# Optimization experiments

Measured on AMD Instinct MI355X. Metric: run time of the kernel, lower is better.

Reference implementation:

```python
import jax, jax.numpy as jnp
import numpy as np

B, H0, W0, C = 8, 56, 56, 256
KC = VC = C
HID = 4 * C
NH = 8  # ChannelAttention default num_heads


def _ln(x, g, b, eps=1e-5):
    m = x.mean(-1, keepdims=True)
    v = jnp.var(x, axis=-1, keepdims=True)
    return (x - m) * jax.lax.rsqrt(v + eps) * g + b


def _dwconv(x, w, b, H, W):
    # x: [B, N, C] -> depthwise 3x3 on [B, C, H, W]
    Bn, N, Cc = x.shape
    t = x.transpose(0, 2, 1).reshape(Bn, Cc, H, W)
    y = jax.lax.conv_general_dilated(t, w, (1, 1), 'SAME', feature_group_count=Cc,
                                     dimension_numbers=('NCHW', 'OIHW', 'NCHW'))
    y = y + b[None, :, None, None]
    return y.reshape(Bn, Cc, H * W).transpose(0, 2, 1)


def _mixffn(x, H, W, w1, b1, dww, dwb, lg, lb, w2, b2):
    f = x @ w1.T + b1  # fc1(x), reused for the skip (torch computes it twice, same value)
    ax = jax.nn.gelu(_ln(_dwconv(f, dww, dwb, H, W) + f, lg, lb), approximate=False)
    return ax @ w2.T + b2


def _eff_attn(xn, kw, kb, qw, qb, vw, vb, rw, rb):
    # 1x1 convs == per-pixel linear; head_count=1
    k = jax.nn.softmax(xn @ kw.T + kb, axis=1)  # softmax over spatial N
    q = jax.nn.softmax(xn @ qw.T + qb, axis=2)  # softmax over key channels
    v = xn @ vw.T + vb
    ctx = jnp.einsum('bnk,bnv->bkv', k, v)      # [B, KC, VC]
    att = jnp.einsum('bkv,bnk->bnv', ctx, q)    # [B, N, VC]
    return att @ rw.T + rb


def _chan_attn(xn, temp, qkv_w, pw, pb):
    Bn, N, Cc = xn.shape
    d = Cc // NH
    qkv = (xn @ qkv_w.T).reshape(Bn, N, 3, NH, d).transpose(2, 0, 3, 4, 1)  # [3,B,h,d,N]
    q, k, v = qkv[0], qkv[1], qkv[2]
    q = q / jnp.maximum(jnp.linalg.norm(q, axis=-1, keepdims=True), 1e-12)
    k = k / jnp.maximum(jnp.linalg.norm(k, axis=-1, keepdims=True), 1e-12)
    attn = jax.nn.softmax(jnp.einsum('bhdn,bhen->bhde', q, k) * temp, axis=-1)  # [B,h,d,d]
    out = jnp.einsum('bhde,bhen->bhdn', attn, v).transpose(0, 3, 1, 2).reshape(Bn, N, Cc)
    return out @ pw.T + pb


def _forward(x, ln1g, ln1b, eakw, eakb, eaqw, eaqb, eavw, eavb, earw, earb,
             ln2g, ln2b, m1w1, m1b1, m1dww, m1dwb, m1lg, m1lb, m1w2, m1b2,
             ln3g, ln3b, catemp, caqkvw, capw, capb,
             ln4g, ln4b, m2w1, m2b1, m2dww, m2dwb, m2lg, m2lb, m2w2, m2b2, H, W):
    add1 = x + _eff_attn(_ln(x, ln1g, ln1b), eakw, eakb, eaqw, eaqb, eavw, eavb, earw, earb)
    add2 = add1 + _mixffn(_ln(add1, ln2g, ln2b), H, W, m1w1, m1b1, m1dww, m1dwb, m1lg, m1lb, m1w2, m1b2)
    add3 = add2 + _chan_attn(_ln(add2, ln3g, ln3b), catemp, caqkvw, capw, capb)
    return add3 + _mixffn(_ln(add3, ln4g, ln4b), H, W, m2w1, m2b1, m2dww, m2dwb, m2lg, m2lb, m2w2, m2b2)


def setup_inputs() -> dict:
    key = jax.random.key(0)
    ks = jax.random.split(key, 16)
    s = 0.02
    rn = lambda k, shape: jax.random.normal(k, shape, jnp.float32) * s
    f32 = jnp.float32
    return {
        'x': jax.random.normal(ks[0], (B, H0 * W0, C), f32),
        'H': H0, 'W': W0,
        'ln1g': jnp.ones(C, f32), 'ln1b': jnp.zeros(C, f32),
        'eakw': rn(ks[1], (KC, C)), 'eakb': jnp.zeros(KC, f32),
        'eaqw': rn(ks[2], (KC, C)), 'eaqb': jnp.zeros(KC, f32),
        'eavw': rn(ks[3], (VC, C)), 'eavb': jnp.zeros(VC, f32),
        'earw': rn(ks[4], (C, VC)), 'earb': jnp.zeros(C, f32),
        'ln2g': jnp.ones(C, f32), 'ln2b': jnp.zeros(C, f32),
        'm1w1': rn(ks[5], (HID, C)), 'm1b1': jnp.zeros(HID, f32),
        'm1dww': rn(ks[6], (HID, 1, 3, 3)), 'm1dwb': jnp.zeros(HID, f32),
        'm1lg': jnp.ones(HID, f32), 'm1lb': jnp.zeros(HID, f32),
        'm1w2': rn(ks[7], (C, HID)), 'm1b2': jnp.zeros(C, f32),
        'ln3g': jnp.ones(C, f32), 'ln3b': jnp.zeros(C, f32),
        'catemp': jnp.ones((NH, 1, 1), f32),
        'caqkvw': rn(ks[8], (3 * C, C)),
        'capw': rn(ks[9], (C, C)), 'capb': jnp.zeros(C, f32),
        'ln4g': jnp.ones(C, f32), 'ln4b': jnp.zeros(C, f32),
        'm2w1': rn(ks[10], (HID, C)), 'm2b1': jnp.zeros(HID, f32),
        'm2dww': rn(ks[11], (HID, 1, 3, 3)), 'm2dwb': jnp.zeros(HID, f32),
        'm2lg': jnp.ones(HID, f32), 'm2lb': jnp.zeros(HID, f32),
        'm2w2': rn(ks[12], (C, HID)), 'm2b2': jnp.zeros(C, f32),
    }


def reference(x, H, W, ln1g, ln1b, eakw, eakb, eaqw, eaqb, eavw, eavb, earw, earb,
              ln2g, ln2b, m1w1, m1b1, m1dww, m1dwb, m1lg, m1lb, m1w2, m1b2,
              ln3g, ln3b, catemp, caqkvw, capw, capb,
              ln4g, ln4b, m2w1, m2b1, m2dww, m2dwb, m2lg, m2lb, m2w2, m2b2):
    return _forward(x, ln1g, ln1b, eakw, eakb, eaqw, eaqb, eavw, eavb, earw, earb,
                    ln2g, ln2b, m1w1, m1b1, m1dww, m1dwb, m1lg, m1lb, m1w2, m1b2,
                    ln3g, ln3b, catemp, caqkvw, capw, capb,
                    ln4g, ln4b, m2w1, m2b1, m2dww, m2dwb, m2lg, m2lb, m2w2, m2b2, H, W)
```

## Files before the change

kernel.cpp:

```cpp
#include <hip/hip_runtime.h>
#include <hip/hip_bf16.h>

typedef __hip_bfloat16 bf16;
typedef __attribute__((ext_vector_type(8))) short short8;
typedef __attribute__((ext_vector_type(4))) float floatx4;

#define DI __device__ __forceinline__

DI unsigned short bfbits(float f){
    bf16 h = __float2bfloat16(f);
    return *reinterpret_cast<unsigned short*>(&h);
}
DI float bu(unsigned short u){
    union { unsigned int i; float f; } x; x.i = ((unsigned int)u) << 16; return x.f;
}

DI float gelu_exact(float x){
    float z = fabsf(x) * 0.70710678118654752f;
    float t = __builtin_amdgcn_rcpf(fmaf(0.3275911f, z, 1.f));
    float p = t * fmaf(t, fmaf(t, fmaf(t, fmaf(t, 1.061405429f, -1.453152027f),
                    1.421413741f), -0.284496736f), 0.254829592f);
    float e = __expf(-z*z);
    float er = fmaf(-p, e, 1.f);
    er = copysignf(er, x);
    return 0.5f * x * (1.f + er);
}

DI void gload16(const void* g, void* l){
    __builtin_amdgcn_global_load_lds(
        (const __attribute__((address_space(1))) unsigned int*)g,
        (__attribute__((address_space(3))) unsigned int*)l,
        16, 0, 0);
}

static constexpr int BATCH = 8;
static constexpr int HH = 56, WW = 56;
static constexpr int NPOS = HH * WW;
static constexpr int CDIM = 256;
static constexpr int HIDD = 1024;
static constexpr int MTOT = BATCH * NPOS;
static constexpr int NCHUNK = 49;
static constexpr int LP = 40;
static constexpr int TNS = 7;

struct WArgs {
    const float* src[10];
    bf16* dst[10];
    int n[10];
};
__global__ __launch_bounds__(256) void wcvt_kernel(WArgs a){
    int wid = blockIdx.y;
    int i = (blockIdx.x*256 + threadIdx.x) * 8;
    if (i >= a.n[wid]) return;
    const float* s = a.src[wid] + i;
    float4 f0 = *(const float4*)(s);
    float4 f1 = *(const float4*)(s + 4);
    union { uint4 u; unsigned short us[8]; } p;
    p.us[0]=bfbits(f0.x); p.us[1]=bfbits(f0.y); p.us[2]=bfbits(f0.z); p.us[3]=bfbits(f0.w);
    p.us[4]=bfbits(f1.x); p.us[5]=bfbits(f1.y); p.us[6]=bfbits(f1.z); p.us[7]=bfbits(f1.w);
    *(uint4*)(a.dst[wid] + i) = p.u;
}

__global__ __launch_bounds__(256) void wtrans_kernel(const float* __restrict__ w1, const float* __restrict__ w2,
                                                     float* __restrict__ t1, float* __restrict__ t2){
    int i = blockIdx.x*256 + threadIdx.x;
    const float* w = blockIdx.y ? w2 : w1;
    float* t = blockIdx.y ? t2 : t1;
    int tap = i >> 10, c = i & 1023;
    t[i] = w[c*9 + tap];
}

template<typename TC>
__global__ __launch_bounds__(256) void mfma_gemm(
    const bf16* __restrict__ A, const bf16* __restrict__ Bw,
    const float* __restrict__ bias, const float* __restrict__ addend,
    TC* __restrict__ C, int M, int N, int K, int lda,
    long long strA, long long strB, long long strC, long long strAdd)
{
    __shared__ __align__(16) float smemf[8192];
    short* S = (short*)smemf;
    int tid = threadIdx.x;
    int bz = blockIdx.z;
    A  += (long long)bz * strA;
    Bw += (long long)bz * strB;
    C  += (long long)bz * strC;
    if (addend) addend += (long long)bz * strAdd;

    int gx = gridDim.x;
    int nwg = gx * gridDim.y;
    int bidl = blockIdx.y * gx + blockIdx.x;
    int qq = nwg >> 3, rr = nwg & 7;
    int xcd = bidl & 7, ixx = bidl >> 3;
    int tile = (xcd < rr) ? (xcd*(qq+1) + ixx) : (rr*(qq+1) + (xcd-rr)*qq + ixx);
    int n0 = (tile % gx) * 128, m0 = (tile / gx) * 128;

    int w = tid >> 6, lane = tid & 63, lm = lane & 15, quad = lane >> 4;
    int mw = (w >> 1) * 64, nw = (w & 1) * 64;

    int c0 = w*128 + lane, c1 = c0 + 64;
    int ar0 = c0 >> 2, ac0 = (c0 & 3) ^ (ar0 & 3);
    int ar1 = c1 >> 2, ac1 = (c1 & 3) ^ (ar1 & 3);
    int rgA0 = m0 + ar0; if (rgA0 > M-1) rgA0 = M-1;
    int rgA1 = m0 + ar1; if (rgA1 > M-1) rgA1 = M-1;
    short* aL0 = S + (2*w+0)*512;
    short* aL1 = S + (2*w+1)*512;
    short* bL0 = S + 4096 + (2*w+0)*512;
    short* bL1 = S + 4096 + (2*w+1)*512;
    const bf16* Arow0 = A + (long long)rgA0*lda + ac0*8;
    const bf16* Arow1 = A + (long long)rgA1*lda + ac1*8;
    const bf16* Brow0 = Bw + (long long)(n0+ar0)*K + ac0*8;
    const bf16* Brow1 = Bw + (long long)(n0+ar1)*K + ac1*8;

    floatx4 z = {0.f, 0.f, 0.f, 0.f};
    floatx4 acc[4][4];
    #pragma unroll
    for (int mi = 0; mi < 4; mi++)
        #pragma unroll
        for (int ni = 0; ni < 4; ni++) acc[mi][ni] = z;

    int sq = quad ^ (lm & 3);

    auto STAGE = [&](int k0, int poff){
        gload16(Arow0 + k0, aL0 + poff);
        gload16(Arow1 + k0, aL1 + poff);
        gload16(Brow0 + k0, bL0 + poff);
        gload16(Brow1 + k0, bL1 + poff);
    };

    STAGE(0, 0);
    __syncthreads();
    int NS = K >> 5;
    for (int st = 0; st < NS; st++){
        int poff = (st & 1) << 13;
        if (st + 1 < NS) STAGE((st+1)*32, poff ^ 8192);
        short8 af[4], bfr[4];
        #pragma unroll
        for (int mi = 0; mi < 4; mi++)
            af[mi] = *(const short8*)&S[poff + (((mw + mi*16 + lm)<<2) + sq)*8];
        #pragma unroll
        for (int ni = 0; ni < 4; ni++)
            bfr[ni] = *(const short8*)&S[poff + 4096 + (((nw + ni*16 + lm)<<2) + sq)*8];
        #pragma unroll
        for (int mi = 0; mi < 4; mi++)
            #pragma unroll
            for (int ni = 0; ni < 4; ni++)
                acc[mi][ni] = __builtin_amdgcn_mfma_f32_16x16x32_bf16(af[mi], bfr[ni], acc[mi][ni], 0, 0, 0);
        __syncthreads();
    }

    float bvv[4];
    #pragma unroll
    for (int ni = 0; ni < 4; ni++)
        bvv[ni] = bias ? bias[n0 + nw + ni*16 + lm] : 0.f;
    float* esc = smemf + w*1088;
    int rl0 = lane >> 3;
    #pragma unroll
    for (int mi = 0; mi < 4; mi++){
        #pragma unroll
        for (int ni = 0; ni < 4; ni++)
            #pragma unroll
            for (int r = 0; r < 4; r++)
                esc[(quad*4 + r)*68 + ni*16 + lm] = acc[mi][ni][r] + bvv[ni];
        #pragma unroll
        for (int p = 0; p < 2; p++){
            int rloc = p*8 + rl0;
            int rg = m0 + mw + mi*16 + rloc;
            if (rg < M){
                if constexpr (sizeof(TC) == 2){
                    int cl = (lane & 7) * 8;
                    float4 u0 = *(const float4*)&esc[rloc*68 + cl];
                    float4 u1 = *(const float4*)&esc[rloc*68 + cl + 4];
                    if (addend){
                        long long ai = (long long)rg*N + (n0 + nw + cl);
                        float4 a0 = *(const float4*)(addend + ai);
                        float4 a1 = *(const float4*)(addend + ai + 4);
                        u0.x+=a0.x; u0.y+=a0.y; u0.z+=a0.z; u0.w+=a0.w;
                        u1.x+=a1.x; u1.y+=a1.y; u1.z+=a1.z; u1.w+=a1.w;
                    }
                    union { uint4 u; unsigned short us[8]; } pk;
                    pk.us[0]=bfbits(u0.x); pk.us[1]=bfbits(u0.y); pk.us[2]=bfbits(u0.z); pk.us[3]=bfbits(u0.w);
                    pk.us[4]=bfbits(u1.x); pk.us[5]=bfbits(u1.y); pk.us[6]=bfbits(u1.z); pk.us[7]=bfbits(u1.w);
                    *(uint4*)(C + (long long)rg*N + (n0 + nw + cl)) = pk.u;
                } else {
                    int cl4 = (lane & 7) * 4;
                    long long co = (long long)rg*N + (n0 + nw);
                    float4 u0 = *(const float4*)&esc[rloc*68 + cl4];
                    float4 u1 = *(const float4*)&esc[rloc*68 + 32 + cl4];
                    if (addend){
                        float4 a0 = *(const float4*)(addend + co + cl4);
                        float4 a1 = *(const float4*)(addend + co + 32 + cl4);
                        u0.x+=a0.x; u0.y+=a0.y; u0.z+=a0.z; u0.w+=a0.w;
                        u1.x+=a1.x; u1.y+=a1.y; u1.z+=a1.z; u1.w+=a1.w;
                    }
                    *(float4*)(C + co + cl4) = u0;
                    *(float4*)(C + co + 32 + cl4) = u1;
                }
            }
        }
    }
}

__global__ __launch_bounds__(256) void gemm_tn_mfma(const bf16* __restrict__ V, const bf16* __restrict__ Kb,
                                                    float* __restrict__ part){
    __shared__ short As[128*LP];
    __shared__ short Bs[128*LP];
    int tid = threadIdx.x;
    int bz = blockIdx.z;
    int b = bz / TNS, s = bz % TNS;
    const bf16* Vb = V  + (long long)b*NPOS*CDIM;
    const bf16* Kc = Kb + (long long)b*NPOS*CDIM;
    int m0 = blockIdx.y * 128, n0 = blockIdx.x * 128;
    int w = tid >> 6, lane = tid & 63, lm = lane & 15, quad = lane >> 4;
    int mw = (w >> 1) * 64, nw = (w & 1) * 64;

    floatx4 z = {0.f,0.f,0.f,0.f};
    floatx4 acc[4][4];
    #pragma unroll
    for (int mi = 0; mi < 4; mi++)
        #pragma unroll
        for (int ni = 0; ni < 4; ni++) acc[mi][ni] = z;

    int r = tid & 31, cgrp = tid >> 5;

    for (int step = 0; step < 448/32; step++){
        int nb = s*448 + step*32;
        #pragma unroll
        for (int cc = 0; cc < 2; cc++){
            int ch = cgrp*8 + cc*64;
            short8 va = *(const short8*)(Vb + (long long)(nb + r)*CDIM + m0 + ch);
            short8 ka = *(const short8*)(Kc + (long long)(nb + r)*CDIM + n0 + ch);
            #pragma unroll
            for (int i = 0; i < 8; i++){
                As[(ch+i)*LP + r] = va[i];
                Bs[(ch+i)*LP + r] = ka[i];
            }
        }
        __syncthreads();
        short8 af[4], bfr[4];
        #pragma unroll
        for (int mi = 0; mi < 4; mi++)
            af[mi] = *(const short8*)&As[(mw + mi*16 + lm)*LP + quad*8];
        #pragma unroll
        for (int ni = 0; ni < 4; ni++)
            bfr[ni] = *(const short8*)&Bs[(nw + ni*16 + lm)*LP + quad*8];
        #pragma unroll
        for (int mi = 0; mi < 4; mi++)
            #pragma unroll
            for (int ni = 0; ni < 4; ni++)
                acc[mi][ni] = __builtin_amdgcn_mfma_f32_16x16x32_bf16(af[mi], bfr[ni], acc[mi][ni], 0, 0, 0);
        __syncthreads();
    }

    float* pb = part + (long long)bz * CDIM * CDIM;
    #pragma unroll
    for (int ni = 0; ni < 4; ni++){
        int cg = n0 + nw + ni*16 + lm;
        #pragma unroll
        for (int mi = 0; mi < 4; mi++){
            #pragma unroll
            for (int rr = 0; rr < 4; rr++){
                int rg = m0 + mw + mi*16 + quad*4 + rr;
                pb[(long long)rg*CDIM + cg] = acc[mi][ni][rr];
            }
        }
    }
}

__global__ __launch_bounds__(256) void ctx_reduce(const float* __restrict__ part, bf16* __restrict__ ctxb){
    long long idx = (long long)blockIdx.x*256 + threadIdx.x;
    int b = (int)(idx >> 16);
    int rem = (int)(idx & 65535);
    float s = 0.f;
    #pragma unroll
    for (int sp = 0; sp < TNS; sp++)
        s += part[((long long)(b*TNS+sp) << 16) + rem];
    ctxb[idx] = __float2bfloat16(s);
}

DI void st4o(float* p, long long i, float a, float b, float c, float d){
    float4 v = make_float4(a,b,c,d); *(float4*)(p + i) = v;
}
DI void st4o(bf16* p, long long i, float a, float b, float c, float d){
    union { unsigned long long u; unsigned short us[4]; } pk;
    pk.us[0]=bfbits(a); pk.us[1]=bfbits(b); pk.us[2]=bfbits(c); pk.us[3]=bfbits(d);
    *(unsigned long long*)(p + i) = pk.u;
}
template<typename TOUT>
__global__ __launch_bounds__(256) void ln4_kernel(const float* __restrict__ x, const float* __restrict__ g,
                                                  const float* __restrict__ b, TOUT* __restrict__ y){
    int wv = threadIdx.x >> 6, lane = threadIdx.x & 63;
    long long row = (long long)blockIdx.x*4 + wv;
    float4 v = *(const float4*)(x + row*256 + lane*4);
    float s  = v.x + v.y + v.z + v.w;
    float ss = v.x*v.x + v.y*v.y + v.z*v.z + v.w*v.w;
    #pragma unroll
    for (int off = 32; off > 0; off >>= 1){
        s  += __shfl_down(s,  off);
        ss += __shfl_down(ss, off);
    }
    s = __shfl(s, 0); ss = __shfl(ss, 0);
    float mean = s * (1.f/256.f);
    float var  = ss * (1.f/256.f) - mean*mean;
    float inv  = rsqrtf(var + 1e-5f);
    float4 gv = *(const float4*)(g + lane*4);
    float4 bv = *(const float4*)(b + lane*4);
    st4o(y, row*256 + lane*4,
         (v.x-mean)*inv*gv.x + bv.x, (v.y-mean)*inv*gv.y + bv.y,
         (v.z-mean)*inv*gv.z + bv.z, (v.w-mean)*inv*gv.w + bv.w);
}

__global__ __launch_bounds__(256) void colsm_p1(const float* __restrict__ x, float* __restrict__ lmax, float* __restrict__ lsum){
    int b = blockIdx.x / NCHUNK, ch = blockIdx.x % NCHUNK;
    int c = threadIdx.x;
    const float* base = x + ((long long)b*NPOS + ch*64)*512 + c;
    float m = -1e30f;
    for (int r = 0; r < 64; r++) m = fmaxf(m, base[(long long)r*512]);
    float s = 0.f;
    for (int r = 0; r < 64; r++) s += expf(base[(long long)r*512] - m);
    lmax[(long long)blockIdx.x*CDIM + c] = m;
    lsum[(long long)blockIdx.x*CDIM + c] = s;
}
__global__ __launch_bounds__(256) void colsm_p2(const float* __restrict__ lmax, const float* __restrict__ lsum,
                                                float* __restrict__ gmax, float* __restrict__ ginv){
    int b = blockIdx.x; int c = threadIdx.x;
    float g = -1e30f;
    for (int ch = 0; ch < NCHUNK; ch++) g = fmaxf(g, lmax[((long long)b*NCHUNK+ch)*CDIM + c]);
    float s = 0.f;
    for (int ch = 0; ch < NCHUNK; ch++)
        s += lsum[((long long)b*NCHUNK+ch)*CDIM + c] * expf(lmax[((long long)b*NCHUNK+ch)*CDIM + c] - g);
    gmax[b*CDIM + c] = g; ginv[b*CDIM + c] = 1.f / s;
}
__global__ __launch_bounds__(256) void colsm_p3(const float* __restrict__ x, bf16* __restrict__ y,
                                                const float* __restrict__ gmax, const float* __restrict__ ginv){
    long long idx = (long long)blockIdx.x*256 + threadIdx.x;
    int c = (int)(idx & 255);
    long long row = idx >> 8;
    int b = (int)(row / NPOS);
    y[idx] = __float2bfloat16(expf(x[row*512 + c] - gmax[b*CDIM + c]) * ginv[b*CDIM + c]);
}

__global__ __launch_bounds__(256) void rowsm4b_kernel(const float* __restrict__ x, const float* __restrict__ bias,
                                                      bf16* __restrict__ y){
    int wv = threadIdx.x >> 6, lane = threadIdx.x & 63;
    long long row = (long long)blockIdx.x*4 + wv;
    float4 v = *(const float4*)(x + row*512 + 256 + lane*4);
    float4 bb = *(const float4*)(bias + lane*4);
    v.x += bb.x; v.y += bb.y; v.z += bb.z; v.w += bb.w;
    float m = fmaxf(fmaxf(v.x, v.y), fmaxf(v.z, v.w));
    #pragma unroll
    for (int off = 32; off > 0; off >>= 1) m = fmaxf(m, __shfl_down(m, off));
    m = __shfl(m, 0);
    float e0 = expf(v.x - m), e1 = expf(v.y - m), e2 = expf(v.z - m), e3 = expf(v.w - m);
    float s = e0 + e1 + e2 + e3;
    #pragma unroll
    for (int off = 32; off > 0; off >>= 1) s += __shfl_down(s, off);
    s = __shfl(s, 0);
    float inv = 1.f / s;
    st4o(y, row*256 + lane*4, e0*inv, e1*inv, e2*inv, e3*inv);
}

__global__ __launch_bounds__(256) void dwconv_ln_gelu_kernel(const bf16* __restrict__ f, const float* __restrict__ wT,
        const float* __restrict__ db, const float* __restrict__ lg, const float* __restrict__ lb, bf16* __restrict__ out){
    __shared__ short Ls[18*1024];
    int tid = threadIdx.x;
    int b = blockIdx.x & 7;
    int rem = blockIdx.x >> 3;
    int h = rem / 14, w0 = (rem % 14) * 4;
    const bf16* fb = f + (long long)b * NPOS * HIDD;

    #pragma unroll
    for (int j = 0; j < 9; j++){
        int idx = j*256 + tid;
        int rc = idx >> 7, chunk = idx & 127;
        int row = rc / 6, col = rc % 6;
        int hy = h - 1 + row, wx = w0 - 1 + col;
        uint4 v = {0,0,0,0};
        if (hy >= 0 && hy < HH && wx >= 0 && wx < WW)
            v = *(const uint4*)(fb + (long long)(hy*WW + wx)*HIDD + chunk*8);
        *(uint4*)&Ls[rc*1024 + chunk*8] = v;
    }
    __syncthreads();

    int ph = tid >> 7, ct = tid & 127;
    int c0 = ct * 8;
    float sv[2][8];
    {
        float4 d0 = *(const float4*)(db + c0);
        float4 d1 = *(const float4*)(db + c0 + 4);
        #pragma unroll
        for (int pp = 0; pp < 2; pp++){
            sv[pp][0]=d0.x; sv[pp][1]=d0.y; sv[pp][2]=d0.z; sv[pp][3]=d0.w;
            sv[pp][4]=d1.x; sv[pp][5]=d1.y; sv[pp][6]=d1.z; sv[pp][7]=d1.w;
        }
    }
    #pragma unroll
    for (int tap = 0; tap < 9; tap++){
        int ky = tap / 3, kx = tap % 3;
        float4 w0v = *(const float4*)(wT + tap*1024 + c0);
        float4 w1v = *(const float4*)(wT + tap*1024 + c0 + 4);
        float wv[8] = {w0v.x,w0v.y,w0v.z,w0v.w,w1v.x,w1v.y,w1v.z,w1v.w};
        #pragma unroll
        for (int pp = 0; pp < 2; pp++){
            int pos_local = 2*ph + pp;
            short8 val = *(const short8*)&Ls[(ky*6 + pos_local + kx)*1024 + c0];
            #pragma unroll
            for (int i = 0; i < 8; i++){
                float fv = bu((unsigned short)val[i]);
                sv[pp][i] += fv * wv[i];
                if (tap == 4) sv[pp][i] += fv;
            }
        }
    }
    float* rr = (float*)Ls;
    __syncthreads();
    #pragma unroll
    for (int pp = 0; pp < 2; pp++){
        float s = 0.f, ss = 0.f;
        #pragma unroll
        for (int i = 0; i < 8; i++){ s += sv[pp][i]; ss += sv[pp][i]*sv[pp][i]; }
        rr[(ph*2+pp)*128 + ct] = s;
        rr[512 + (ph*2+pp)*128 + ct] = ss;
    }
    __syncthreads();
    {
        int wv = tid >> 6, ln = tid & 63;
        float s  = rr[wv*128 + ln]       + rr[wv*128 + ln + 64];
        float ss = rr[512 + wv*128 + ln] + rr[512 + wv*128 + ln + 64];
        #pragma unroll
        for (int off = 32; off > 0; off >>= 1){
            s  += __shfl_down(s,  off);
            ss += __shfl_down(ss, off);
        }
        if (ln == 0){ rr[1024 + wv] = s; rr[1028 + wv] = ss; }
    }
    __syncthreads();
    float4 g0 = *(const float4*)(lg + c0), g1 = *(const float4*)(lg + c0 + 4);
    float4 b0 = *(const float4*)(lb + c0), b1 = *(const float4*)(lb + c0 + 4);
    float gg[8] = {g0.x,g0.y,g0.z,g0.w,g1.x,g1.y,g1.z,g1.w};
    float bb[8] = {b0.x,b0.y,b0.z,b0.w,b1.x,b1.y,b1.z,b1.w};
    #pragma unroll
    for (int pp = 0; pp < 2; pp++){
        int pos_local = 2*ph + pp;
        long long n = (long long)b*NPOS + h*WW + (w0 + pos_local);
        float mean = rr[1024 + ph*2+pp] * (1.f/HIDD);
        float var  = rr[1028 + ph*2+pp] * (1.f/HIDD) - mean*mean;
        float inv  = rsqrtf(var + 1e-5f);
        union { uint4 u; unsigned short us[8]; } ov;
        #pragma unroll
        for (int i = 0; i < 8; i++){
            float o = (sv[pp][i]-mean)*inv*gg[i] + bb[i];
            ov.us[i] = bfbits(gelu_exact(o));
        }
        *(uint4*)(out + n*HIDD + c0) = ov.u;
    }
}

__global__ __launch_bounds__(256) void ssq_p1(const bf16* __restrict__ qkv, float* __restrict__ lss){
    __shared__ float red[4][64][8];
    int b = blockIdx.x / NCHUNK, ch = blockIdx.x % NCHUNK;
    int tid = threadIdx.x;
    int col = (tid & 63) * 8;
    int rg = tid >> 6;
    float s[8] = {0,0,0,0,0,0,0,0};
    for (int r = rg*16; r < rg*16 + 16; r++){
        long long row = (long long)(b*NPOS + ch*64 + r);
        union { uint4 u; unsigned short us[8]; } v;
        v.u = *(const uint4*)(qkv + row*768 + col);
        #pragma unroll
        for (int i = 0; i < 8; i++){ float f = bu(v.us[i]); s[i] += f*f; }
    }
    #pragma unroll
    for (int i = 0; i < 8; i++) red[rg][tid & 63][i] = s[i];
    __syncthreads();
    if (tid < 64){
        #pragma unroll
        for (int i = 0; i < 8; i++){
            float t = red[0][tid][i] + red[1][tid][i] + red[2][tid][i] + red[3][tid][i];
            lss[(long long)blockIdx.x*512 + tid*8 + i] = t;
        }
    }
}
__global__ __launch_bounds__(256) void ssq_p2(const float* __restrict__ lss, float* __restrict__ invn){
    int b = blockIdx.x; int c = blockIdx.y*256 + threadIdx.x;
    float s = 0.f;
    for (int ch = 0; ch < NCHUNK; ch++) s += lss[((long long)b*NCHUNK+ch)*512 + c];
    invn[b*512 + c] = 1.f / fmaxf(sqrtf(s), 1e-12f);
}

__global__ __launch_bounds__(256) void chanattn_qk_part(const bf16* __restrict__ qkv, const float* __restrict__ invn,
                                                        float* __restrict__ part){
    __shared__ float qs[64][36];
    __shared__ float ks[64][36];
    int bz = blockIdx.x;
    int bh = bz / TNS, s = bz % TNS;
    int b = bh >> 3, hh = bh & 7;
    int tid = threadIdx.x;
    int d = tid >> 3, e0 = (tid & 7) * 4;
    int sr = tid >> 2, sc8 = (tid & 3) * 8;
    float invq[8], invk[8];
    {
        float4 a0 = *(const float4*)(invn + b*512 + hh*32 + sc8);
        float4 a1 = *(const float4*)(invn + b*512 + hh*32 + sc8 + 4);
        float4 b0 = *(const float4*)(invn + b*512 + 256 + hh*32 + sc8);
        float4 b1 = *(const float4*)(invn + b*512 + 256 + hh*32 + sc8 + 4);
        invq[0]=a0.x; invq[1]=a0.y; invq[2]=a0.z; invq[3]=a0.w;
        invq[4]=a1.x; invq[5]=a1.y; invq[6]=a1.z; invq[7]=a1.w;
        invk[0]=b0.x; invk[1]=b0.y; invk[2]=b0.z; invk[3]=b0.w;
        invk[4]=b1.x; invk[5]=b1.y; invk[6]=b1.z; invk[7]=b1.w;
    }
    float acc[4] = {0.f,0.f,0.f,0.f};
    for (int it = 0; it < 7; it++){
        int n0 = s*448 + it*64;
        {
            long long rowb = (long long)(b*NPOS + n0 + sr) * 768;
            union { uint4 u; unsigned short us[8]; } qv, kv;
            qv.u = *(const uint4*)(qkv + rowb + hh*32 + sc8);
            kv.u = *(const uint4*)(qkv + rowb + 256 + hh*32 + sc8);
            #pragma unroll
            for (int i = 0; i < 8; i++){
                qs[sr][sc8+i] = bu(qv.us[i]) * invq[i];
                ks[sr][sc8+i] = bu(kv.us[i]) * invk[i];
            }
        }
        __syncthreads();
        #pragma unroll 4
        for (int r = 0; r < 64; r++){
            float qv = qs[r][d];
            #pragma unroll
            for (int j = 0; j < 4; j++) acc[j] += qv * ks[r][e0+j];
        }
        __syncthreads();
    }
    #pragma unroll
    for (int j = 0; j < 4; j++)
        part[(long long)bz*1024 + d*32 + e0 + j] = acc[j];
}
__global__ __launch_bounds__(256) void chanattn_qk_fin(const float* __restrict__ part, const float* __restrict__ temp,
                                                       float* __restrict__ attn){
    __shared__ float att_s[32][33];
    int bh = blockIdx.x;
    int hh = bh & 7;
    int tid = threadIdx.x;
    int d = tid >> 3, e0 = (tid & 7) * 4;
    float t = temp[hh];
    #pragma unroll
    for (int j = 0; j < 4; j++){
        float s = 0.f;
        for (int sp = 0; sp < TNS; sp++)
            s += part[((long long)bh*TNS + sp)*1024 + d*32 + e0 + j];
        att_s[d][e0+j] = s * t;
    }
    __syncthreads();
    if (tid < 32){
        float m = -1e30f;
        for (int e = 0; e < 32; e++) m = fmaxf(m, att_s[tid][e]);
        float s = 0.f;
        for (int e = 0; e < 32; e++){ float ev = expf(att_s[tid][e] - m); att_s[tid][e] = ev; s += ev; }
        float inv = 1.f / s;
        for (int e = 0; e < 32; e++) att_s[tid][e] *= inv;
    }
    __syncthreads();
    #pragma unroll
    for (int j = 0; j < 4; j++)
        attn[(long long)bh*1024 + d*32 + e0 + j] = att_s[d][e0+j];
}

__global__ __launch_bounds__(256) void wcomb_kernel(const float* __restrict__ capw, const float* __restrict__ attn,
                                                    bf16* __restrict__ Wb){
    __shared__ float at_s[8192];
    int b = blockIdx.x, og = blockIdx.y;
    int tid = threadIdx.x;
    #pragma unroll
    for (int j = 0; j < 8; j++)
        *(float4*)&at_s[tid*32 + j*4] = *(const float4*)(attn + (long long)b*8192 + tid*32 + j*4);
    __syncthreads();
    int o = og*32 + (tid & 31);
    int h = tid >> 5;
    float acc[32];
    #pragma unroll
    for (int e = 0; e < 32; e++) acc[e] = 0.f;
    for (int d = 0; d < 32; d++){
        float w = capw[(long long)o*256 + h*32 + d];
        const float* ar = &at_s[h*1024 + d*32];
        #pragma unroll
        for (int eq = 0; eq < 8; eq++){
            float4 av = *(const float4*)(ar + eq*4);
            acc[eq*4+0] += w*av.x; acc[eq*4+1] += w*av.y;
            acc[eq*4+2] += w*av.z; acc[eq*4+3] += w*av.w;
        }
    }
    bf16* dst = Wb + (long long)b*65536 + (long long)o*256 + h*32;
    #pragma unroll
    for (int eq = 0; eq < 4; eq++){
        union { uint4 u; unsigned short us[8]; } p;
        #pragma unroll
        for (int i = 0; i < 8; i++) p.us[i] = bfbits(acc[eq*8+i]);
        *(uint4*)(dst + eq*8) = p.u;
    }
}

extern "C" void kernel_launch(void* const* d_in, const int* in_sizes, int n_in,
                              void* d_out, int out_size, void* d_ws, size_t ws_size,
                              hipStream_t stream){
    const float* x     = (const float*)d_in[0];
    const float* ln1g  = (const float*)d_in[3];
    const float* ln1b  = (const float*)d_in[4];
    const float* eakw  = (const float*)d_in[5];
    const float* eaqw  = (const float*)d_in[7];
    const float* eaqb  = (const float*)d_in[8];
    const float* eavw  = (const float*)d_in[9];
    const float* eavb  = (const float*)d_in[10];
    const float* earw  = (const float*)d_in[11];
    const float* earb  = (const float*)d_in[12];
    const float* ln2g  = (const float*)d_in[13];
    const float* ln2b  = (const float*)d_in[14];
    const float* m1w1  = (const float*)d_in[15];
    const float* m1b1  = (const float*)d_in[16];
    const float* m1dww = (const float*)d_in[17];
    const float* m1dwb = (const float*)d_in[18];
    const float* m1lg  = (const float*)d_in[19];
    const float* m1lb  = (const float*)d_in[20];
    const float* m1w2  = (const float*)d_in[21];
    const float* m1b2  = (const float*)d_in[22];
    const float* ln3g  = (const float*)d_in[23];
    const float* ln3b  = (const float*)d_in[24];
    const float* catemp= (const float*)d_in[25];
    const float* caqkvw= (const float*)d_in[26];
    const float* capw  = (const float*)d_in[27];
    const float* capb  = (const float*)d_in[28];
    const float* ln4g  = (const float*)d_in[29];
    const float* ln4b  = (const float*)d_in[30];
    const float* m2w1  = (const float*)d_in[31];
    const float* m2b1  = (const float*)d_in[32];
    const float* m2dww = (const float*)d_in[33];
    const float* m2dwb = (const float*)d_in[34];
    const float* m2lg  = (const float*)d_in[35];
    const float* m2lb  = (const float*)d_in[36];
    const float* m2w2  = (const float*)d_in[37];
    const float* m2b2  = (const float*)d_in[38];

    char* base = (char*)d_ws;
    auto alloc = [&](size_t nbytes){ char* p = base; base += (nbytes + 255) & ~(size_t)255; return p; };
    constexpr size_t SZ = (size_t)MTOT*CDIM*4;
    float* R  = (float*)alloc(SZ);
    float* A0 = (float*)alloc(SZ);
    float* A1 = (float*)alloc(SZ);
    float* B0 = (float*)alloc(SZ);
    float* B1 = (float*)alloc(SZ);
    bf16* A0b  = (bf16*)A0;
    bf16* kb   = (bf16*)A0;
    bf16* qb   = A0b + (size_t)MTOT*CDIM;
    bf16* vb   = (bf16*)A1;
    float* KQ  = B0;
    bf16* attb = (bf16*)B0;
    bf16* l2b  = (bf16*)A1;
    bf16* F    = (bf16*)B0;
    bf16* G    = (bf16*)A0;
    bf16* l3b  = (bf16*)B0;
    bf16* Qb   = (bf16*)A0;
    bf16* l4b  = (bf16*)A0;
    bf16* ctxb = (bf16*)alloc((size_t)BATCH*CDIM*CDIM*2);
    float* lmax = (float*)alloc((size_t)BATCH*NCHUNK*CDIM*4);
    float* lsum = (float*)alloc((size_t)BATCH*NCHUNK*CDIM*4);
    float* gmax = (float*)alloc((size_t)BATCH*CDIM*4);
    float* ginv = (float*)alloc((size_t)BATCH*CDIM*4);
    float* lss  = (float*)alloc((size_t)BATCH*NCHUNK*512*4);
    float* invn = (float*)alloc((size_t)BATCH*512*4);
    float* attnb= (float*)alloc((size_t)BATCH*8*32*32*4);
    float* ptn  = (float*)alloc((size_t)BATCH*TNS*CDIM*CDIM*4);
    float* pqk  = (float*)alloc((size_t)BATCH*8*TNS*1024*4);
    bf16* wbuf  = (bf16*)alloc((size_t)1572864*2);
    float* wT1  = (float*)alloc((size_t)9216*4);
    float* wT2  = (float*)alloc((size_t)9216*4);
    bf16* Wcb   = (bf16*)alloc((size_t)BATCH*CDIM*CDIM*2);

    bf16* kqw_b    = wbuf;
    bf16* eavw_b   = wbuf + 131072;
    bf16* earw_b   = wbuf + 196608;
    bf16* m1w1_b   = wbuf + 262144;
    bf16* m1w2_b   = wbuf + 524288;
    bf16* caqkvw_b = wbuf + 786432;
    bf16* m2w1_b   = wbuf + 1048576;
    bf16* m2w2_b   = wbuf + 1310720;

    dim3 blk(256);
    constexpr int MB = MTOT/128;
    long long sA1 = (long long)NPOS*CDIM;
    long long sB1 = (long long)CDIM*CDIM;

    {
        WArgs wa;
        const float* srcs[10] = {eakw, eaqw, eavw, earw, m1w1, m1w2, caqkvw, m2w1, m2w2, m2w2};
        bf16* dsts[10] = {kqw_b, kqw_b + 65536, eavw_b, earw_b, m1w1_b, m1w2_b, caqkvw_b, m2w1_b, m2w2_b, m2w2_b};
        int ns[10] = {65536, 65536, 65536, 65536, 262144, 262144, 196608, 262144, 262144, 0};
        for (int i = 0; i < 10; i++){ wa.src[i]=srcs[i]; wa.dst[i]=dsts[i]; wa.n[i]=ns[i]; }
        wcvt_kernel<<<dim3(128,10), blk, 0, stream>>>(wa);
        wtrans_kernel<<<dim3(36,2), blk, 0, stream>>>(m1dww, m2dww, wT1, wT2);
    }

    ln4_kernel<bf16><<<MTOT/4, blk, 0, stream>>>(x, ln1g, ln1b, A0b);
    mfma_gemm<float><<<dim3(4,MB,1), blk, 0, stream>>>(A0b, kqw_b, nullptr, nullptr, KQ, MTOT, 512, 256, 256, 0,0,0,0);
    mfma_gemm<bf16><<<dim3(2,MB,1), blk, 0, stream>>>(A0b, eavw_b, eavb, nullptr, vb, MTOT, 256, 256, 256, 0,0,0,0);
    rowsm4b_kernel<<<MTOT/4, blk, 0, stream>>>(KQ, eaqb, qb);
    colsm_p1<<<BATCH*NCHUNK, blk, 0, stream>>>(KQ, lmax, lsum);
    colsm_p2<<<BATCH, blk, 0, stream>>>(lmax, lsum, gmax, ginv);
    colsm_p3<<<MTOT, blk, 0, stream>>>(KQ, kb, gmax, ginv);
    gemm_tn_mfma<<<dim3(2,2,BATCH*TNS), blk, 0, stream>>>(vb, kb, ptn);
    ctx_reduce<<<(BATCH*65536)/256, blk, 0, stream>>>(ptn, ctxb);
    mfma_gemm<bf16><<<dim3(2,25,BATCH), blk, 0, stream>>>(qb, ctxb, nullptr, nullptr, attb,
            NPOS, 256, 256, 256, sA1, sB1, sA1, 0);
    mfma_gemm<float><<<dim3(2,MB,1), blk, 0, stream>>>(attb, earw_b, earb, x, R, MTOT, 256, 256, 256, 0,0,0,0);

    ln4_kernel<bf16><<<MTOT/4, blk, 0, stream>>>(R, ln2g, ln2b, l2b);
    mfma_gemm<bf16><<<dim3(8,MB,1), blk, 0, stream>>>(l2b, m1w1_b, m1b1, nullptr, F, MTOT, 1024, 256, 256, 0,0,0,0);
    dwconv_ln_gelu_kernel<<<BATCH*HH*14, blk, 0, stream>>>(F, wT1, m1dwb, m1lg, m1lb, G);
    mfma_gemm<float><<<dim3(2,MB,1), blk, 0, stream>>>(G, m1w2_b, m1b2, R, R, MTOT, 256, 1024, 1024, 0,0,0,0);

    ln4_kernel<bf16><<<MTOT/4, blk, 0, stream>>>(R, ln3g, ln3b, l3b);
    mfma_gemm<bf16><<<dim3(6,MB,1), blk, 0, stream>>>(l3b, caqkvw_b, nullptr, nullptr, Qb, MTOT, 768, 256, 256, 0,0,0,0);
    ssq_p1<<<BATCH*NCHUNK, blk, 0, stream>>>(Qb, lss);
    ssq_p2<<<dim3(BATCH,2), blk, 0, stream>>>(lss, invn);
    chanattn_qk_part<<<BATCH*8*TNS, blk, 0, stream>>>(Qb, invn, pqk);
    chanattn_qk_fin<<<BATCH*8, blk, 0, stream>>>(pqk, catemp, attnb);
    wcomb_kernel<<<dim3(BATCH,8), blk, 0, stream>>>(capw, attnb, Wcb);
    mfma_gemm<float><<<dim3(2,25,BATCH), blk, 0, stream>>>(Qb + 512, Wcb, capb, R, R,
            NPOS, 256, 256, 768, (long long)NPOS*768, sB1, sA1, sA1);

    ln4_kernel<bf16><<<MTOT/4, blk, 0, stream>>>(R, ln4g, ln4b, l4b);
    mfma_gemm<bf16><<<dim3(8,MB,1), blk, 0, stream>>>(l4b, m2w1_b, m2b1, nullptr, F, MTOT, 1024, 256, 256, 0,0,0,0);
    dwconv_ln_gelu_kernel<<<BATCH*HH*14, blk, 0, stream>>>(F, wT2, m2dwb, m2lg, m2lb, G);
    mfma_gemm<float><<<dim3(2,MB,1), blk, 0, stream>>>(G, m2w2_b, m2b2, R, (float*)d_out, MTOT, 256, 1024, 1024, 0,0,0,0);
}
```

Before: 566.0 us.

## Fuse key/query softmax kernels and rewrite depthwise conv to register sliding window

Merges the row softmax for queries and the final column-softmax normalization for keys into one kernel, so one launch covers both and the row-major reads of KQ happen in a single pass. Separately, the depthwise 3x3 conv drops its shared-memory halo staging: each thread loads a 3x4 window of inputs straight from global memory into registers and reuses it for two adjacent output pixels. Interior blocks take a branch-free path, while border blocks clamp their indices and zero-mask the out-of-range inputs. This removes the LDS traffic and a barrier, but more global loads now overlap between neighbouring threads and blocks, and the kernel relies on cache hits for that reuse.

```diff
diff --git a/kernel.cpp b/kernel.cpp
--- a/kernel.cpp
+++ b/kernel.cpp
@@ -330,19 +330,13 @@
         s += lsum[((long long)b*NCHUNK+ch)*CDIM + c] * expf(lmax[((long long)b*NCHUNK+ch)*CDIM + c] - g);
     gmax[b*CDIM + c] = g; ginv[b*CDIM + c] = 1.f / s;
 }
-__global__ __launch_bounds__(256) void colsm_p3(const float* __restrict__ x, bf16* __restrict__ y,
-                                                const float* __restrict__ gmax, const float* __restrict__ ginv){
-    long long idx = (long long)blockIdx.x*256 + threadIdx.x;
-    int c = (int)(idx & 255);
-    long long row = idx >> 8;
-    int b = (int)(row / NPOS);
-    y[idx] = __float2bfloat16(expf(x[row*512 + c] - gmax[b*CDIM + c]) * ginv[b*CDIM + c]);
-}
-
-__global__ __launch_bounds__(256) void rowsm4b_kernel(const float* __restrict__ x, const float* __restrict__ bias,
-                                                      bf16* __restrict__ y){
+
+__global__ __launch_bounds__(256) void kqsm_kernel(const float* __restrict__ x, const float* __restrict__ bias,
+                                                   const float* __restrict__ gmax, const float* __restrict__ ginv,
+                                                   bf16* __restrict__ kb, bf16* __restrict__ qb){
     int wv = threadIdx.x >> 6, lane = threadIdx.x & 63;
     long long row = (long long)blockIdx.x*4 + wv;
+    int b = blockIdx.x / 784;
     float4 v = *(const float4*)(x + row*512 + 256 + lane*4);
     float4 bb = *(const float4*)(bias + lane*4);
     v.x += bb.x; v.y += bb.y; v.z += bb.z; v.w += bb.w;
@@ -356,82 +350,101 @@
     for (int off = 32; off > 0; off >>= 1) s += __shfl_down(s, off);
     s = __shfl(s, 0);
     float inv = 1.f / s;
-    st4o(y, row*256 + lane*4, e0*inv, e1*inv, e2*inv, e3*inv);
+    st4o(qb, row*256 + lane*4, e0*inv, e1*inv, e2*inv, e3*inv);
+    float4 kv = *(const float4*)(x + row*512 + lane*4);
+    float4 gm = *(const float4*)(gmax + b*CDIM + lane*4);
+    float4 gi = *(const float4*)(ginv + b*CDIM + lane*4);
+    st4o(kb, row*256 + lane*4,
+         expf(kv.x - gm.x)*gi.x, expf(kv.y - gm.y)*gi.y,
+         expf(kv.z - gm.z)*gi.z, expf(kv.w - gm.w)*gi.w);
+}
+
+template<bool G>
+DI void conv_core(const bf16* __restrict__ fb, const float* __restrict__ wT,
+                  int h, int pw, int c0, float* acc0, float* acc1){
+    #pragma unroll
+    for (int r = 0; r < 3; r++){
+        int hy = h - 1 + r;
+        bool rv = !G || (hy >= 0 && hy < HH);
+        int hyc = G ? min(max(hy, 0), HH-1) : hy;
+        float u[4][8];
+        #pragma unroll
+        for (int c = 0; c < 4; c++){
+            int wx = pw - 1 + c;
+            bool vv = rv && (!G || (wx >= 0 && wx < WW));
+            int wxc = G ? min(max(wx, 0), WW-1) : wx;
+            uint4 raw = *(const uint4*)(fb + (long long)(hyc*WW + wxc)*HIDD + c0);
+            unsigned short* us = (unsigned short*)&raw;
+            #pragma unroll
+            for (int i = 0; i < 8; i++){
+                float xv = bu(us[i]);
+                u[c][i] = (G && !vv) ? 0.f : xv;
+            }
+        }
+        #pragma unroll
+        for (int kx = 0; kx < 3; kx++){
+            float4 wA = *(const float4*)(wT + (r*3+kx)*1024 + c0);
+            float4 wB = *(const float4*)(wT + (r*3+kx)*1024 + c0 + 4);
+            float wv[8] = {wA.x,wA.y,wA.z,wA.w,wB.x,wB.y,wB.z,wB.w};
+            #pragma unroll
+            for (int i = 0; i < 8; i++){
+                acc0[i] = fmaf(u[kx][i],   wv[i], acc0[i]);
+                acc1[i] = fmaf(u[kx+1][i], wv[i], acc1[i]);
+            }
+        }
+        if (r == 1){
+            #pragma unroll
+            for (int i = 0; i < 8; i++){ acc0[i] += u[1][i]; acc1[i] += u[2][i]; }
+        }
+    }
 }
 
 __global__ __launch_bounds__(256) void dwconv_ln_gelu_kernel(const bf16* __restrict__ f, const float* __restrict__ wT,
         const float* __restrict__ db, const float* __restrict__ lg, const float* __restrict__ lb, bf16* __restrict__ out){
-    __shared__ short Ls[18*1024];
+    __shared__ float rs[4][128], rq[4][128], rfin[8];
     int tid = threadIdx.x;
     int b = blockIdx.x & 7;
     int rem = blockIdx.x >> 3;
     int h = rem / 14, w0 = (rem % 14) * 4;
     const bf16* fb = f + (long long)b * NPOS * HIDD;
-
-    #pragma unroll
-    for (int j = 0; j < 9; j++){
-        int idx = j*256 + tid;
-        int rc = idx >> 7, chunk = idx & 127;
-        int row = rc / 6, col = rc % 6;
-        int hy = h - 1 + row, wx = w0 - 1 + col;
-        uint4 v = {0,0,0,0};
-        if (hy >= 0 && hy < HH && wx >= 0 && wx < WW)
-            v = *(const uint4*)(fb + (long long)(hy*WW + wx)*HIDD + chunk*8);
-        *(uint4*)&Ls[rc*1024 + chunk*8] = v;
-    }
-    __syncthreads();
-
     int ph = tid >> 7, ct = tid & 127;
     int c0 = ct * 8;
-    float sv[2][8];
+    int pw = w0 + 2*ph;
+
+    float acc0[8], acc1[8];
     {
         float4 d0 = *(const float4*)(db + c0);
         float4 d1 = *(const float4*)(db + c0 + 4);
-        #pragma unroll
-        for (int pp = 0; pp < 2; pp++){
-            sv[pp][0]=d0.x; sv[pp][1]=d0.y; sv[pp][2]=d0.z; sv[pp][3]=d0.w;
-            sv[pp][4]=d1.x; sv[pp][5]=d1.y; sv[pp][6]=d1.z; sv[pp][7]=d1.w;
-        }
-    }
-    #pragma unroll
-    for (int tap = 0; tap < 9; tap++){
-        int ky = tap / 3, kx = tap % 3;
-        float4 w0v = *(const float4*)(wT + tap*1024 + c0);
-        float4 w1v = *(const float4*)(wT + tap*1024 + c0 + 4);
-        float wv[8] = {w0v.x,w0v.y,w0v.z,w0v.w,w1v.x,w1v.y,w1v.z,w1v.w};
-        #pragma unroll
-        for (int pp = 0; pp < 2; pp++){
-            int pos_local = 2*ph + pp;
-            short8 val = *(const short8*)&Ls[(ky*6 + pos_local + kx)*1024 + c0];
-            #pragma unroll
-            for (int i = 0; i < 8; i++){
-                float fv = bu((unsigned short)val[i]);
-                sv[pp][i] += fv * wv[i];
-                if (tap == 4) sv[pp][i] += fv;
-            }
-        }
-    }
-    float* rr = (float*)Ls;
-    __syncthreads();
-    #pragma unroll
-    for (int pp = 0; pp < 2; pp++){
-        float s = 0.f, ss = 0.f;
-        #pragma unroll
-        for (int i = 0; i < 8; i++){ s += sv[pp][i]; ss += sv[pp][i]*sv[pp][i]; }
-        rr[(ph*2+pp)*128 + ct] = s;
-        rr[512 + (ph*2+pp)*128 + ct] = ss;
+        acc0[0]=d0.x; acc0[1]=d0.y; acc0[2]=d0.z; acc0[3]=d0.w;
+        acc0[4]=d1.x; acc0[5]=d1.y; acc0[6]=d1.z; acc0[7]=d1.w;
+        #pragma unroll
+        for (int i = 0; i < 8; i++) acc1[i] = acc0[i];
+    }
+    bool interior = (h > 0) && (h < HH-1) && (w0 > 0) && (w0 < 52);
+    if (interior) conv_core<false>(fb, wT, h, pw, c0, acc0, acc1);
+    else          conv_core<true >(fb, wT, h, pw, c0, acc0, acc1);
+
+    {
+        float s0=0.f, q0=0.f, s1=0.f, q1=0.f;
+        #pragma unroll
+        for (int i = 0; i < 8; i++){
+            s0 += acc0[i]; q0 += acc0[i]*acc0[i];
+            s1 += acc1[i]; q1 += acc1[i]*acc1[i];
+        }
+        rs[2*ph][ct] = s0; rq[2*ph][ct] = q0;
+        rs[2*ph+1][ct] = s1; rq[2*ph+1][ct] = q1;
     }
     __syncthreads();
     {
         int wv = tid >> 6, ln = tid & 63;
-        float s  = rr[wv*128 + ln]       + rr[wv*128 + ln + 64];
-        float ss = rr[512 + wv*128 + ln] + rr[512 + wv*128 + ln + 64];
+        float s = rs[wv][ln] + rs[wv][ln+64];
+        float q = rq[wv][ln] + rq[wv][ln+64];
         #pragma unroll
         for (int off = 32; off > 0; off >>= 1){
-            s  += __shfl_down(s,  off);
-            ss += __shfl_down(ss, off);
-        }
-        if (ln == 0){ rr[1024 + wv] = s; rr[1028 + wv] = ss; }
+            s += __shfl_down(s, off);
+            q += __shfl_down(q, off);
+        }
+        if (ln == 0){ rfin[wv] = s; rfin[4+wv] = q; }
     }
     __syncthreads();
     float4 g0 = *(const float4*)(lg + c0), g1 = *(const float4*)(lg + c0 + 4);
@@ -440,15 +453,16 @@
     float bb[8] = {b0.x,b0.y,b0.z,b0.w,b1.x,b1.y,b1.z,b1.w};
     #pragma unroll
     for (int pp = 0; pp < 2; pp++){
-        int pos_local = 2*ph + pp;
-        long long n = (long long)b*NPOS + h*WW + (w0 + pos_local);
-        float mean = rr[1024 + ph*2+pp] * (1.f/HIDD);
-        float var  = rr[1028 + ph*2+pp] * (1.f/HIDD) - mean*mean;
+        int g = 2*ph + pp;
+        long long n = (long long)b*NPOS + h*WW + (pw + pp);
+        float mean = rfin[g] * (1.f/HIDD);
+        float var  = rfin[4+g] * (1.f/HIDD) - mean*mean;
         float inv  = rsqrtf(var + 1e-5f);
+        const float* ac = pp ? acc1 : acc0;
         union { uint4 u; unsigned short us[8]; } ov;
         #pragma unroll
         for (int i = 0; i < 8; i++){
-            float o = (sv[pp][i]-mean)*inv*gg[i] + bb[i];
+            float o = (ac[i]-mean)*inv*gg[i] + bb[i];
             ov.us[i] = bfbits(gelu_exact(o));
         }
         *(uint4*)(out + n*HIDD + c0) = ov.u;
@@ -701,10 +715,9 @@
     ln4_kernel<bf16><<<MTOT/4, blk, 0, stream>>>(x, ln1g, ln1b, A0b);
     mfma_gemm<float><<<dim3(4,MB,1), blk, 0, stream>>>(A0b, kqw_b, nullptr, nullptr, KQ, MTOT, 512, 256, 256, 0,0,0,0);
     mfma_gemm<bf16><<<dim3(2,MB,1), blk, 0, stream>>>(A0b, eavw_b, eavb, nullptr, vb, MTOT, 256, 256, 256, 0,0,0,0);
-    rowsm4b_kernel<<<MTOT/4, blk, 0, stream>>>(KQ, eaqb, qb);
     colsm_p1<<<BATCH*NCHUNK, blk, 0, stream>>>(KQ, lmax, lsum);
     colsm_p2<<<BATCH, blk, 0, stream>>>(lmax, lsum, gmax, ginv);
-    colsm_p3<<<MTOT, blk, 0, stream>>>(KQ, kb, gmax, ginv);
+    kqsm_kernel<<<MTOT/4, blk, 0, stream>>>(KQ, eaqb, gmax, ginv, kb, qb);
     gemm_tn_mfma<<<dim3(2,2,BATCH*TNS), blk, 0, stream>>>(vb, kb, ptn);
     ctx_reduce<<<(BATCH*65536)/256, blk, 0, stream>>>(ptn, ctxb);
     mfma_gemm<bf16><<<dim3(2,25,BATCH), blk, 0, stream>>>(qb, ctxb, nullptr, nullptr, attb,
```

New measurement: 551.5 us. 1.03x faster.
